# Kernel optimization log

Measured on AMD Instinct MI355X. Metric: run time of the kernel, lower is better.

## Reference

```python
import jax, jax.numpy as jnp
import numpy as np

B, T, I, H, O = 4096, 200, 2, 64, 2


def setup_inputs() -> dict:
    key = jax.random.key(0)
    ks = jax.random.split(key, 7)
    s = 1.0 / np.sqrt(H)  # PyTorch LSTM init scale
    return {
        "x": jax.random.normal(ks[0], (B, T, I), dtype=jnp.float32),
        "W_ih": jax.random.uniform(ks[1], (4 * H, I), jnp.float32, -s, s),
        "W_hh": jax.random.uniform(ks[2], (4 * H, H), jnp.float32, -s, s),
        "b_ih": jax.random.uniform(ks[3], (4 * H,), jnp.float32, -s, s),
        "b_hh": jax.random.uniform(ks[4], (4 * H,), jnp.float32, -s, s),
        "W_fc": jax.random.uniform(ks[5], (O, H), jnp.float32, -s, s),
        "b_fc": jax.random.uniform(ks[6], (O,), jnp.float32, -s, s),
    }


def reference(x, W_ih, W_hh, b_ih, b_hh, W_fc, b_fc):
    # Precompute input-to-gate projections for all timesteps in one GEMM.
    # xg: [T, B, 4H] (time-major for scan)
    xg = jnp.einsum("bti,gi->tbg", x, W_ih) + (b_ih + b_hh)

    def step(carry, xt):
        h, c = carry  # [B, H] each
        gates = xt + h @ W_hh.T  # [B, 4H]
        i_g, f_g, g_g, o_g = jnp.split(gates, 4, axis=-1)  # PyTorch order: i, f, g, o
        i = jax.nn.sigmoid(i_g)
        f = jax.nn.sigmoid(f_g)
        g = jnp.tanh(g_g)
        o = jax.nn.sigmoid(o_g)
        c = f * c + i * g
        h = o * jnp.tanh(c)
        return (h, c), None

    h0 = jnp.zeros((x.shape[0], W_hh.shape[1]), dtype=x.dtype)
    c0 = jnp.zeros_like(h0)
    (h_last, _), _ = jax.lax.scan(step, (h0, c0), xg)
    return h_last @ W_fc.T + b_fc  # [B, O]
```

## Files before the change

kernel.cpp:

```cpp
#include <hip/hip_runtime.h>
#include <hip/hip_bf16.h>


#define B_ 4096
#define T_ 200

typedef _Float16 half8 __attribute__((ext_vector_type(8)));
typedef float f32x4 __attribute__((ext_vector_type(4)));

#define K1f 1.4426950408889634f
#define K2f 2.8853900817779268f

__global__ __launch_bounds__(512) void lstm_kernel(
    const float* __restrict__ x,
    const float* __restrict__ W_ih,
    const float* __restrict__ W_hh,
    const float* __restrict__ b_ih,
    const float* __restrict__ b_hh,
    const float* __restrict__ W_fc,
    const float* __restrict__ b_fc,
    float* __restrict__ out)
{
    __shared__ float xs[16][404];
    __shared__ _Float16 h16[2][16][72];
    __shared__ float wfc[130];

    const int tid  = threadIdx.x;
    const int lane = tid & 63;
    const int w    = tid >> 6;
    const int wq   = w & 3;
    const int half = w >> 2;
    const int cidx = lane & 15;
    const int grp  = lane >> 4;
    const int r0   = blockIdx.x * 16;

    for (int i4 = tid; i4 < 1600; i4 += 512) {
        const int row = i4 / 100;
        const int j4  = i4 - row * 100;
        reinterpret_cast<float4*>(&xs[row][0])[j4] =
            reinterpret_cast<const float4*>(x + (size_t)(r0 + row) * 400)[j4];
    }
    for (int i = tid; i < 1152; i += 512)
        reinterpret_cast<unsigned int*>(&h16[0][0][0])[i] = 0u;
    if (tid < 130) wfc[tid] = (tid < 128) ? W_fc[tid] : b_fc[tid - 128];

    half8 bfrag[4][2];
    float wi0[4], wi1[4], bs[4];
    const int u = wq * 16 + cidx;
    #pragma unroll
    for (int m = 0; m < 4; ++m) {
        const float sc = (m == 2) ? K2f : -K1f;
        const int g = m * 64 + u;
        wi0[m] = W_ih[g * 2 + 0] * sc;
        wi1[m] = W_ih[g * 2 + 1] * sc;
        bs[m]  = (b_ih[g] + b_hh[g]) * sc;
        #pragma unroll
        for (int kt = 0; kt < 2; ++kt) {
            const float* p = W_hh + g * 64 + kt * 32 + grp * 8;
            const float4 lo = reinterpret_cast<const float4*>(p)[0];
            const float4 hi = reinterpret_cast<const float4*>(p)[1];
            half8 f;
            f[0] = (_Float16)(lo.x * sc); f[1] = (_Float16)(lo.y * sc);
            f[2] = (_Float16)(lo.z * sc); f[3] = (_Float16)(lo.w * sc);
            f[4] = (_Float16)(hi.x * sc); f[5] = (_Float16)(hi.y * sc);
            f[6] = (_Float16)(hi.z * sc); f[7] = (_Float16)(hi.w * sc);
            bfrag[m][kt] = f;
        }
    }

    const int arow = (cidx + 2 * half) & 15;
    const int rowA = grp * 4 + 2 * half;
    float cstA = 0.f, cstB = 0.f;

    __syncthreads();

    #define ACT(pi, pf, pg, po, cst, hvout)                                    \
        {                                                                      \
            const float Ei = __builtin_amdgcn_exp2f(pi);                       \
            const float Ef = __builtin_amdgcn_exp2f(pf);                       \
            const float Eg = __builtin_amdgcn_exp2f(pg);                       \
            const float Eo = __builtin_amdgcn_exp2f(po);                       \
            const float fEf = 1.0f + Ef;                                       \
            const float P   = (1.0f + Ei) * (Eg + 1.0f);                       \
            const float r1  = __builtin_amdgcn_rcpf(P * fEf);                  \
            cst = fmaf(cst, P, (Eg - 1.0f) * fEf) * r1;                        \
            const float Ec = __builtin_amdgcn_exp2f(fminf(K2f * cst, 60.0f));  \
            const float r2 = __builtin_amdgcn_rcpf((1.0f + Eo) * (Ec + 1.0f)); \
            hvout = (Ec - 1.0f) * r2;                                          \
        }

    float projA[4], projB[4];
    {
        const float2 xvA = *reinterpret_cast<const float2*>(&xs[rowA][0]);
        const float2 xvB = *reinterpret_cast<const float2*>(&xs[rowA + 1][0]);
        #pragma unroll
        for (int m = 0; m < 4; ++m) {
            projA[m] = fmaf(xvA.y, wi1[m], fmaf(xvA.x, wi0[m], bs[m]));
            projB[m] = fmaf(xvB.y, wi1[m], fmaf(xvB.x, wi0[m], bs[m]));
        }
    }

    #pragma unroll 2
    for (int t = 0; t < T_; ++t) {
        const int rd = t & 1;
        const _Float16* hb = &h16[rd][0][0];
        const half8 a0 = *reinterpret_cast<const half8*>(hb + arow * 72 + grp * 8);
        const half8 a1 = *reinterpret_cast<const half8*>(hb + arow * 72 + 32 + grp * 8);

        f32x4 acc[4];
        #pragma unroll
        for (int m = 0; m < 4; ++m) {
            f32x4 c = {projA[m], projB[m], projA[m], projB[m]};
            c = __builtin_amdgcn_mfma_f32_16x16x32_f16(a0, bfrag[m][0], c, 0, 0, 0);
            c = __builtin_amdgcn_mfma_f32_16x16x32_f16(a1, bfrag[m][1], c, 0, 0, 0);
            acc[m] = c;
        }

        {
            const float2 xvA = *reinterpret_cast<const float2*>(&xs[rowA][2 * t + 2]);
            const float2 xvB = *reinterpret_cast<const float2*>(&xs[rowA + 1][2 * t + 2]);
            #pragma unroll
            for (int m = 0; m < 4; ++m) {
                projA[m] = fmaf(xvA.y, wi1[m], fmaf(xvA.x, wi0[m], bs[m]));
                projB[m] = fmaf(xvB.y, wi1[m], fmaf(xvB.x, wi0[m], bs[m]));
            }
        }

        float hvA, hvB;
        ACT(acc[0][0], acc[1][0], acc[2][0], acc[3][0], cstA, hvA);
        ACT(acc[0][1], acc[1][1], acc[2][1], acc[3][1], cstB, hvB);

        h16[rd ^ 1][rowA][u]     = (_Float16)hvA;
        h16[rd ^ 1][rowA + 1][u] = (_Float16)hvB;
        __syncthreads();
    }

    if (tid < 32) {
        const int r = tid & 15;
        const int o = tid >> 4;
        float s = wfc[128 + o];
        #pragma unroll
        for (int k = 0; k < 64; ++k)
            s = fmaf(wfc[o * 64 + k], (float)h16[0][r][k], s);
        out[(size_t)(r0 + r) * 2 + o] = s;
    }
}

extern "C" void kernel_launch(void* const* d_in, const int* in_sizes, int n_in,
                              void* d_out, int out_size, void* d_ws, size_t ws_size,
                              hipStream_t stream) {
    const float* x    = (const float*)d_in[0];
    const float* W_ih = (const float*)d_in[1];
    const float* W_hh = (const float*)d_in[2];
    const float* b_ih = (const float*)d_in[3];
    const float* b_hh = (const float*)d_in[4];
    const float* W_fc = (const float*)d_in[5];
    const float* b_fc = (const float*)d_in[6];
    float* out = (float*)d_out;

    lstm_kernel<<<B_ / 16, 512, 0, stream>>>(x, W_ih, W_hh, b_ih, b_hh, W_fc, b_fc, out);
}
```

Measured before the change: 104.5 us.

## Split batch tile into two interleaved half-groups to overlap recurrence stages

The 16 batch rows per block become two independent 8-row groups (hA and hB) that are advanced alternately within each timestep. Each half-step runs the MFMAs for one group while the other group's activations and h write-back complete, with a barrier after each half. The intent is to hide MFMA and activation latency across two independent recurrences and to give each thread one activation per phase instead of two. In exchange, each MFMA now carries only 8 useful rows, so matrix work doubles, barriers per timestep double, and the loop is no longer unrolled by 2.

```diff
diff --git a/kernel.cpp b/kernel.cpp
--- a/kernel.cpp
+++ b/kernel.cpp
@@ -22,7 +22,8 @@
     float* __restrict__ out)
 {
     __shared__ float xs[16][404];
-    __shared__ _Float16 h16[2][16][72];
+    __shared__ _Float16 hA[8][80];
+    __shared__ _Float16 hB[8][80];
     __shared__ float wfc[130];
 
     const int tid  = threadIdx.x;
@@ -40,8 +41,10 @@
         reinterpret_cast<float4*>(&xs[row][0])[j4] =
             reinterpret_cast<const float4*>(x + (size_t)(r0 + row) * 400)[j4];
     }
-    for (int i = tid; i < 1152; i += 512)
-        reinterpret_cast<unsigned int*>(&h16[0][0][0])[i] = 0u;
+    for (int i = tid; i < 320; i += 512)
+        reinterpret_cast<unsigned int*>(&hA[0][0])[i] = 0u;
+    for (int i = tid; i < 320; i += 512)
+        reinterpret_cast<unsigned int*>(&hB[0][0])[i] = 0u;
     if (tid < 130) wfc[tid] = (tid < 128) ? W_fc[tid] : b_fc[tid - 128];
 
     half8 bfrag[4][2];
@@ -68,8 +71,8 @@
         }
     }
 
-    const int arow = (cidx + 2 * half) & 15;
-    const int rowA = grp * 4 + 2 * half;
+    const int arow = ((cidx >> 1) + half) & 7;
+    const int rowL = 2 * grp + half;
     float cstA = 0.f, cstB = 0.f;
 
     __syncthreads();
@@ -89,59 +92,74 @@
             hvout = (Ec - 1.0f) * r2;                                          \
         }
 
+    half8 aA0 = {0, 0, 0, 0, 0, 0, 0, 0}, aA1 = {0, 0, 0, 0, 0, 0, 0, 0};
+    half8 aB0, aB1;
+
     float projA[4], projB[4];
     {
-        const float2 xvA = *reinterpret_cast<const float2*>(&xs[rowA][0]);
-        const float2 xvB = *reinterpret_cast<const float2*>(&xs[rowA + 1][0]);
+        const float2 xv = *reinterpret_cast<const float2*>(&xs[rowL][0]);
         #pragma unroll
-        for (int m = 0; m < 4; ++m) {
-            projA[m] = fmaf(xvA.y, wi1[m], fmaf(xvA.x, wi0[m], bs[m]));
-            projB[m] = fmaf(xvB.y, wi1[m], fmaf(xvB.x, wi0[m], bs[m]));
-        }
+        for (int m = 0; m < 4; ++m)
+            projA[m] = fmaf(xv.y, wi1[m], fmaf(xv.x, wi0[m], bs[m]));
     }
 
-    #pragma unroll 2
     for (int t = 0; t < T_; ++t) {
-        const int rd = t & 1;
-        const _Float16* hb = &h16[rd][0][0];
-        const half8 a0 = *reinterpret_cast<const half8*>(hb + arow * 72 + grp * 8);
-        const half8 a1 = *reinterpret_cast<const half8*>(hb + arow * 72 + 32 + grp * 8);
+        aB0 = *reinterpret_cast<const half8*>(&hB[arow][grp * 8]);
+        aB1 = *reinterpret_cast<const half8*>(&hB[arow][32 + grp * 8]);
 
         f32x4 acc[4];
         #pragma unroll
         for (int m = 0; m < 4; ++m) {
-            f32x4 c = {projA[m], projB[m], projA[m], projB[m]};
-            c = __builtin_amdgcn_mfma_f32_16x16x32_f16(a0, bfrag[m][0], c, 0, 0, 0);
-            c = __builtin_amdgcn_mfma_f32_16x16x32_f16(a1, bfrag[m][1], c, 0, 0, 0);
+            f32x4 c = {projA[m], projA[m], projA[m], projA[m]};
+            c = __builtin_amdgcn_mfma_f32_16x16x32_f16(aA0, bfrag[m][0], c, 0, 0, 0);
+            c = __builtin_amdgcn_mfma_f32_16x16x32_f16(aA1, bfrag[m][1], c, 0, 0, 0);
             acc[m] = c;
         }
+        {
+            const float2 xv = *reinterpret_cast<const float2*>(&xs[8 + rowL][2 * t]);
+            #pragma unroll
+            for (int m = 0; m < 4; ++m)
+                projB[m] = fmaf(xv.y, wi1[m], fmaf(xv.x, wi0[m], bs[m]));
+        }
+        {
+            float hv;
+            ACT(acc[0][0], acc[1][0], acc[2][0], acc[3][0], cstA, hv);
+            hA[rowL][u] = (_Float16)hv;
+        }
+        __syncthreads();
 
+        aA0 = *reinterpret_cast<const half8*>(&hA[arow][grp * 8]);
+        aA1 = *reinterpret_cast<const half8*>(&hA[arow][32 + grp * 8]);
+
+        #pragma unroll
+        for (int m = 0; m < 4; ++m) {
+            f32x4 c = {projB[m], projB[m], projB[m], projB[m]};
+            c = __builtin_amdgcn_mfma_f32_16x16x32_f16(aB0, bfrag[m][0], c, 0, 0, 0);
+            c = __builtin_amdgcn_mfma_f32_16x16x32_f16(aB1, bfrag[m][1], c, 0, 0, 0);
+            acc[m] = c;
+        }
         {
-            const float2 xvA = *reinterpret_cast<const float2*>(&xs[rowA][2 * t + 2]);
-            const float2 xvB = *reinterpret_cast<const float2*>(&xs[rowA + 1][2 * t + 2]);
+            const float2 xv = *reinterpret_cast<const float2*>(&xs[rowL][2 * t + 2]);
             #pragma unroll
-            for (int m = 0; m < 4; ++m) {
-                projA[m] = fmaf(xvA.y, wi1[m], fmaf(xvA.x, wi0[m], bs[m]));
-                projB[m] = fmaf(xvB.y, wi1[m], fmaf(xvB.x, wi0[m], bs[m]));
-            }
+            for (int m = 0; m < 4; ++m)
+                projA[m] = fmaf(xv.y, wi1[m], fmaf(xv.x, wi0[m], bs[m]));
         }
-
-        float hvA, hvB;
-        ACT(acc[0][0], acc[1][0], acc[2][0], acc[3][0], cstA, hvA);
-        ACT(acc[0][1], acc[1][1], acc[2][1], acc[3][1], cstB, hvB);
-
-        h16[rd ^ 1][rowA][u]     = (_Float16)hvA;
-        h16[rd ^ 1][rowA + 1][u] = (_Float16)hvB;
+        {
+            float hv;
+            ACT(acc[0][0], acc[1][0], acc[2][0], acc[3][0], cstB, hv);
+            hB[rowL][u] = (_Float16)hv;
+        }
         __syncthreads();
     }
 
     if (tid < 32) {
         const int r = tid & 15;
         const int o = tid >> 4;
+        const _Float16* hsrc = (r < 8) ? &hA[r][0] : &hB[r - 8][0];
         float s = wfc[128 + o];
         #pragma unroll
         for (int k = 0; k < 64; ++k)
-            s = fmaf(wfc[o * 64 + k], (float)h16[0][r][k], s);
+            s = fmaf(wfc[o * 64 + k], (float)hsrc[k], s);
         out[(size_t)(r0 + r) * 2 + o] = s;
     }
 }
```

Measured after the change: 138.2 us. +32.2%, slower.

## Split batch rows into two wave groups with staggered MFMA/activation phases

Applied to the files above, without the earlier changes.

Splits the 16 batch rows into two independent 8-row sub-batches, each handled by four waves. The two groups run out of phase: one group issues its MFMA gate GEMM while the other computes the transcendental activations, with a barrier between phases. The goal is to overlap matrix-core work with ALU/SFU work across waves rather than running them in sequence. The cost is two barriers per timestep instead of one, and each MFMA now uses only 8 of its 16 rows (a0 rows are duplicated), so half the matrix throughput is wasted.

```diff
diff --git a/kernel.cpp b/kernel.cpp
--- a/kernel.cpp
+++ b/kernel.cpp
@@ -22,14 +22,14 @@
     float* __restrict__ out)
 {
     __shared__ float xs[16][404];
-    __shared__ _Float16 h16[2][16][72];
+    __shared__ _Float16 hA[8][72];
+    __shared__ _Float16 hB[8][72];
     __shared__ float wfc[130];
 
     const int tid  = threadIdx.x;
     const int lane = tid & 63;
     const int w    = tid >> 6;
     const int wq   = w & 3;
-    const int half = w >> 2;
     const int cidx = lane & 15;
     const int grp  = lane >> 4;
     const int r0   = blockIdx.x * 16;
@@ -40,8 +40,11 @@
         reinterpret_cast<float4*>(&xs[row][0])[j4] =
             reinterpret_cast<const float4*>(x + (size_t)(r0 + row) * 400)[j4];
     }
-    for (int i = tid; i < 1152; i += 512)
-        reinterpret_cast<unsigned int*>(&h16[0][0][0])[i] = 0u;
+    if (tid < 64) xs[tid >> 2][400 + (tid & 3)] = 0.f;
+    for (int i = tid; i < 288; i += 512)
+        reinterpret_cast<unsigned int*>(&hA[0][0])[i] = 0u;
+    for (int i = tid; i < 288; i += 512)
+        reinterpret_cast<unsigned int*>(&hB[0][0])[i] = 0u;
     if (tid < 130) wfc[tid] = (tid < 128) ? W_fc[tid] : b_fc[tid - 128];
 
     half8 bfrag[4][2];
@@ -68,9 +71,10 @@
         }
     }
 
-    const int arow = (cidx + 2 * half) & 15;
-    const int rowA = grp * 4 + 2 * half;
-    float cstA = 0.f, cstB = 0.f;
+    const int arow = cidx >> 1;
+    const int rowL = 2 * grp;
+    float cst0 = 0.f, cst1 = 0.f;
+    f32x4 acc[4];
 
     __syncthreads();
 
@@ -89,59 +93,59 @@
             hvout = (Ec - 1.0f) * r2;                                          \
         }
 
-    float projA[4], projB[4];
-    {
-        const float2 xvA = *reinterpret_cast<const float2*>(&xs[rowA][0]);
-        const float2 xvB = *reinterpret_cast<const float2*>(&xs[rowA + 1][0]);
-        #pragma unroll
-        for (int m = 0; m < 4; ++m) {
-            projA[m] = fmaf(xvA.y, wi1[m], fmaf(xvA.x, wi0[m], bs[m]));
-            projB[m] = fmaf(xvB.y, wi1[m], fmaf(xvB.x, wi0[m], bs[m]));
-        }
-    }
-
-    #pragma unroll 2
-    for (int t = 0; t < T_; ++t) {
-        const int rd = t & 1;
-        const _Float16* hb = &h16[rd][0][0];
-        const half8 a0 = *reinterpret_cast<const half8*>(hb + arow * 72 + grp * 8);
-        const half8 a1 = *reinterpret_cast<const half8*>(hb + arow * 72 + 32 + grp * 8);
-
-        f32x4 acc[4];
-        #pragma unroll
-        for (int m = 0; m < 4; ++m) {
-            f32x4 c = {projA[m], projB[m], projA[m], projB[m]};
-            c = __builtin_amdgcn_mfma_f32_16x16x32_f16(a0, bfrag[m][0], c, 0, 0, 0);
-            c = __builtin_amdgcn_mfma_f32_16x16x32_f16(a1, bfrag[m][1], c, 0, 0, 0);
-            acc[m] = c;
+    #define PHASE0(hX, gbase, t)                                               \
+        {                                                                      \
+            const half8 a0 = *reinterpret_cast<const half8*>(&hX[arow][grp * 8]);      \
+            const half8 a1 = *reinterpret_cast<const half8*>(&hX[arow][32 + grp * 8]); \
+            const float2 xv0 = *reinterpret_cast<const float2*>(&xs[(gbase) + rowL][2 * (t)]);     \
+            const float2 xv1 = *reinterpret_cast<const float2*>(&xs[(gbase) + rowL + 1][2 * (t)]); \
+            _Pragma("unroll")                                                  \
+            for (int m = 0; m < 4; ++m) {                                      \
+                const float p0 = fmaf(xv0.y, wi1[m], fmaf(xv0.x, wi0[m], bs[m])); \
+                const float p1 = fmaf(xv1.y, wi1[m], fmaf(xv1.x, wi0[m], bs[m])); \
+                f32x4 c = {p0, p0, p1, p1};                                    \
+                c = __builtin_amdgcn_mfma_f32_16x16x32_f16(a0, bfrag[m][0], c, 0, 0, 0); \
+                c = __builtin_amdgcn_mfma_f32_16x16x32_f16(a1, bfrag[m][1], c, 0, 0, 0); \
+                acc[m] = c;                                                    \
+            }                                                                  \
         }
 
-        {
-            const float2 xvA = *reinterpret_cast<const float2*>(&xs[rowA][2 * t + 2]);
-            const float2 xvB = *reinterpret_cast<const float2*>(&xs[rowA + 1][2 * t + 2]);
-            #pragma unroll
-            for (int m = 0; m < 4; ++m) {
-                projA[m] = fmaf(xvA.y, wi1[m], fmaf(xvA.x, wi0[m], bs[m]));
-                projB[m] = fmaf(xvB.y, wi1[m], fmaf(xvB.x, wi0[m], bs[m]));
-            }
+    #define PHASE1(hX)                                                         \
+        {                                                                      \
+            float hv0, hv1;                                                    \
+            ACT(acc[0][0], acc[1][0], acc[2][0], acc[3][0], cst0, hv0);        \
+            ACT(acc[0][2], acc[1][2], acc[2][2], acc[3][2], cst1, hv1);        \
+            hX[rowL][u]     = (_Float16)hv0;                                   \
+            hX[rowL + 1][u] = (_Float16)hv1;                                   \
         }
 
-        float hvA, hvB;
-        ACT(acc[0][0], acc[1][0], acc[2][0], acc[3][0], cstA, hvA);
-        ACT(acc[0][1], acc[1][1], acc[2][1], acc[3][1], cstB, hvB);
-
-        h16[rd ^ 1][rowA][u]     = (_Float16)hvA;
-        h16[rd ^ 1][rowA + 1][u] = (_Float16)hvB;
+    if (w < 4) {
+        PHASE0(hA, 0, 0);
         __syncthreads();
+        for (int t = 0; t < T_; ++t) {
+            PHASE1(hA);
+            __syncthreads();
+            PHASE0(hA, 0, t + 1);
+            __syncthreads();
+        }
+    } else {
+        __syncthreads();
+        for (int t = 0; t < T_; ++t) {
+            PHASE0(hB, 8, t);
+            __syncthreads();
+            PHASE1(hB);
+            __syncthreads();
+        }
     }
 
     if (tid < 32) {
         const int r = tid & 15;
         const int o = tid >> 4;
+        const _Float16* hsrc = (r < 8) ? &hA[r][0] : &hB[r - 8][0];
         float s = wfc[128 + o];
         #pragma unroll
         for (int k = 0; k < 64; ++k)
-            s = fmaf(wfc[o * 64 + k], (float)h16[0][r][k], s);
+            s = fmaf(wfc[o * 64 + k], (float)hsrc[k], s);
         out[(size_t)(r0 + r) * 2 + o] = s;
     }
 }
```

Measured after the change: 119.5 us. 1.14x slower.
